# Optimization experiments

Measured on AMD Instinct MI355X. Metric: run time of the kernel, lower is better.

## Reference

```python
import jax, jax.numpy as jnp
import numpy as np

B, L, N, P = 64, 512, 321, 720   # batch, seq_len, enc_in, pred_len
E, R, CID, H = 8, 32, 32, 64     # experts, rank, channel_identity_dim, router hidden


def setup_inputs() -> dict:
    key = jax.random.key(0)
    ks = jax.random.split(key, 9)
    return {
        "x": jax.random.normal(ks[0], (B, L, N), dtype=jnp.float32),
        # per-channel identity embedding for the router
        "ident": jax.random.normal(ks[1], (N, CID), dtype=jnp.float32) * 0.02,
        # router MLP: CID -> H -> E
        "rw1": jax.random.normal(ks[2], (CID, H), dtype=jnp.float32) * (1.0 / np.sqrt(CID)),
        "rb1": jnp.zeros((H,), dtype=jnp.float32),
        "rw2": jax.random.normal(ks[3], (H, E), dtype=jnp.float32) * (1.0 / np.sqrt(H)),
        "rb2": jnp.zeros((E,), dtype=jnp.float32),
        # low-rank experts: L -> R -> P
        "w1": jax.random.normal(ks[4], (E, L, R), dtype=jnp.float32) * (1.0 / np.sqrt(L)),
        "w2": jax.random.normal(ks[5], (E, R, P), dtype=jnp.float32) * (1.0 / np.sqrt(R)),
        "b": jnp.zeros((E, P), dtype=jnp.float32),
    }


def reference(x, ident, rw1, rb1, rw2, rb2, w1, w2, b):
    # RevIN-style normalization over the time dim (torch std is unbiased, ddof=1)
    mean = jnp.mean(x, axis=1, keepdims=True)                    # [B,1,N]
    std = jnp.std(x, axis=1, keepdims=True, ddof=1) + 1e-6       # [B,1,N]
    xn = ((x - mean) / std).transpose(0, 2, 1)                   # [B,N,L]

    # per-channel MoE router (soft routing over experts)
    hidden = jax.nn.relu(ident @ rw1 + rb1)                      # [N,H]
    gate = jax.nn.softmax(hidden @ rw2 + rb2, axis=-1)           # [N,E]

    # low-rank expert projections L -> R -> P
    h = jnp.einsum('bnl,elr->bner', xn, w1)                      # [B,N,E,R]
    y = jnp.einsum('bner,erp->bnep', h, w2) + b                  # [B,N,E,P]
    y = jnp.einsum('bnep,ne->bnp', y, gate)                      # [B,N,P]

    pred = y.transpose(0, 2, 1)                                  # [B,P,N]
    return pred * std + mean
```

## Files before the change

kernel.cpp:

```cpp
#include <hip/hip_runtime.h>
#include <math.h>

#define B_ 64
#define L_ 512
#define N_ 321
#define P_ 720
#define E_ 8
#define R_ 32
#define CID_ 32
#define H_ 64
#define ER_ 256
#define KB2 288
#define HGROWS 384

typedef __attribute__((ext_vector_type(8))) short bf16x8;
typedef __attribute__((ext_vector_type(4))) float f32x4;
typedef __attribute__((ext_vector_type(8))) unsigned short u16x8;
typedef __attribute__((ext_vector_type(4))) unsigned short u16x4;

#define OFF_GATE 0
#define OFF_CS1  (N_*E_)
#define OFF_W1K  (OFF_CS1 + ER_)
#define OFF_W2X  (OFF_W1K + ER_*L_/2)
#define OFF_HG   (OFF_W2X + P_*KB2/2)

__device__ __forceinline__ unsigned short f2bf(float f) {
    unsigned u = __float_as_uint(f);
    u += 0x7fffu + ((u >> 16) & 1u);
    return (unsigned short)(u >> 16);
}
__device__ __forceinline__ float bf2f(unsigned short h) {
    return __uint_as_float(((unsigned)h) << 16);
}

__global__ void router_kernel(const float* __restrict__ ident,
                              const float* __restrict__ rw1, const float* __restrict__ rb1,
                              const float* __restrict__ rw2, const float* __restrict__ rb2,
                              float* __restrict__ gate) {
    int n = blockIdx.x;
    int t = threadIdx.x;
    __shared__ float hid[H_];
    __shared__ float lg[E_];
    float acc = rb1[t];
    #pragma unroll
    for (int c = 0; c < CID_; ++c)
        acc = fmaf(ident[n*CID_ + c], rw1[c*H_ + t], acc);
    hid[t] = fmaxf(acc, 0.f);
    __syncthreads();
    if (t < E_) {
        float a = rb2[t];
        #pragma unroll
        for (int h = 0; h < H_; ++h) a = fmaf(hid[h], rw2[h*E_ + t], a);
        lg[t] = a;
    }
    __syncthreads();
    if (t == 0) {
        float m = lg[0];
        #pragma unroll
        for (int e = 1; e < E_; ++e) m = fmaxf(m, lg[e]);
        float s = 0.f, ex[E_];
        #pragma unroll
        for (int e = 0; e < E_; ++e) { ex[e] = expf(lg[e] - m); s += ex[e]; }
        float inv = 1.f / s;
        #pragma unroll
        for (int e = 0; e < E_; ++e) gate[n*E_ + e] = ex[e] * inv;
    }
}

__global__ void prep_kernel(const float* __restrict__ w1, const float* __restrict__ w2,
                            const float* __restrict__ bias,
                            unsigned short* __restrict__ w1k, unsigned short* __restrict__ w2x,
                            float* __restrict__ cs1) {
    __shared__ float red[16][32];
    int bid = blockIdx.x, t = threadIdx.x;
    if (bid < 256) {
        int g = bid*512 + t;
        int er = g >> 9, l = g & 511;
        w1k[g] = f2bf(w1[(size_t)(er >> 5)*(L_*R_) + (size_t)l*R_ + (er & 31)]);
    } else if (bid < 256 + 720) {
        int p = bid - 256;
        if (t < KB2) {
            unsigned short v;
            if (t < ER_)            v = f2bf(w2[(size_t)t*P_ + p]);
            else if (t < ER_ + E_)  v = f2bf(bias[(size_t)(t - ER_)*P_ + p]);
            else if (t == ER_ + E_) v = 0x3f80;
            else                    v = 0;
            w2x[(size_t)p*KB2 + t] = v;
        }
    } else {
        int e = bid - 976;
        int q = t >> 5, r = t & 31;
        float s = 0.f;
        for (int l = q; l < L_; l += 16)
            s += bf2f(f2bf(w1[(size_t)e*(L_*R_) + (size_t)l*R_ + r]));
        red[q][r] = s;
        __syncthreads();
        if (q == 0) {
            #pragma unroll
            for (int qq = 1; qq < 16; ++qq) s += red[qq][r];
            cs1[e*32 + r] = s;
        }
    }
}

#define SM_XT   0
#define SM_RED  65536
#define SM_MSD  (65536+4096)
#define SM_TOT  (65536+4096+512)

__global__ __launch_bounds__(512, 4) void gemm1_kernel(
        const float* __restrict__ x, const unsigned short* __restrict__ w1k,
        const float* __restrict__ gate, const float* __restrict__ cs1,
        unsigned short* __restrict__ hg) {
    __shared__ __align__(16) char smem[SM_TOT];
    char* xTc   = smem + SM_XT;
    float* red1 = (float*)(smem + SM_RED);
    float* red2 = red1 + 512;
    float* meanS = (float*)(smem + SM_MSD);
    float* sdS   = meanS + 64;

    const int bid = blockIdx.x;
    const int xcd = bid & 7;
    const int idx = bid >> 3;
    const int b   = (xcd << 3) + idx / 6;
    const int n0  = (idx % 6) * 64;

    const int tid  = threadIdx.x;
    const int lane = tid & 63;
    const int wave = tid >> 6;
    const int l15  = lane & 15;
    const int kgrp = lane >> 4;

    const int xn = tid & 63;
    const int ks8 = tid >> 6;
    const float* xb = x + (size_t)b * L_ * N_;
    const int gn = n0 + xn;
    const bool nvalid = (gn < N_);
    const int xsw = (xn & 7) << 4;

    float s1 = 0.f, s2 = 0.f;
    #pragma unroll
    for (int c8 = 0; c8 < 8; ++c8) {
        const int k0 = ks8*64 + c8*8;
        float v[8];
        #pragma unroll
        for (int j = 0; j < 8; ++j)
            v[j] = nvalid ? xb[(size_t)(k0 + j)*N_ + gn] : 0.f;
        u16x8 pk;
        #pragma unroll
        for (int j = 0; j < 8; ++j) {
            s1 += v[j]; s2 = fmaf(v[j], v[j], s2); pk[j] = f2bf(v[j]);
        }
        *(u16x8*)(xTc + xn*1024 + ((k0*2) ^ xsw)) = pk;
    }
    red1[ks8*64 + xn] = s1;
    red2[ks8*64 + xn] = s2;
    __syncthreads();

    if (tid < 64) {
        float a = 0.f, q = 0.f;
        #pragma unroll
        for (int kk = 0; kk < 8; ++kk) { a += red1[kk*64 + tid]; q += red2[kk*64 + tid]; }
        float mean = a * (1.f/L_);
        float var = (q - (float)L_*mean*mean) * (1.f/(L_-1));
        var = fmaxf(var, 0.f);
        meanS[tid] = mean;
        sdS[tid]   = sqrtf(var) + 1e-6f;
    }
    __syncthreads();

    const unsigned short* apA = w1k + (size_t)(wave*32 + l15)*L_;
    const unsigned short* apB = w1k + (size_t)(wave*32 + 16 + l15)*L_;
    const int rsw = (l15 & 7) << 4;

    f32x4 acc[2][4];
    #pragma unroll
    for (int i = 0; i < 2; ++i)
        #pragma unroll
        for (int j = 0; j < 4; ++j) acc[i][j] = (f32x4){0.f,0.f,0.f,0.f};

    bf16x8 af[4][2];
#define LDA(s_, ks_) { af[s_][0] = *(const bf16x8*)&apA[(ks_)*32 + kgrp*8];      \
                       af[s_][1] = *(const bf16x8*)&apB[(ks_)*32 + kgrp*8]; }
    LDA(0, 0); LDA(1, 1); LDA(2, 2);
    #pragma unroll
    for (int ks = 0; ks < 16; ++ks) {
        if (ks + 3 < 16) LDA((ks + 3) & 3, ks + 3);
        const int cur = ks & 3;
        const int kb = (ks*32 + kgrp*8) * 2;
        #pragma unroll
        for (int fn = 0; fn < 4; ++fn) {
            bf16x8 bfr = *(const bf16x8*)(xTc + (fn*16 + l15)*1024 + (kb ^ rsw));
            acc[0][fn] = __builtin_amdgcn_mfma_f32_16x16x32_bf16(af[cur][0], bfr, acc[0][fn], 0, 0, 0);
            acc[1][fn] = __builtin_amdgcn_mfma_f32_16x16x32_bf16(af[cur][1], bfr, acc[1][fn], 0, 0, 0);
        }
    }
#undef LDA

    unsigned short* hgb = hg + ((size_t)b * HGROWS + n0) * KB2;
    #pragma unroll
    for (int fm = 0; fm < 2; ++fm) {
        int er0 = wave*32 + fm*16 + kgrp*4;
        int e = er0 >> 5;
        f32x4 c4 = *(const f32x4*)&cs1[er0];
        #pragma unroll
        for (int fn = 0; fn < 4; ++fn) {
            int nl = fn*16 + l15;
            int gnn = n0 + nl; if (gnn > N_-1) gnn = N_-1;
            float g = gate[gnn*E_ + e];
            float m = meanS[nl];
            u16x4 pk;
            #pragma unroll
            for (int j = 0; j < 4; ++j)
                pk[j] = f2bf(g * (acc[fm][fn][j] - m * c4[j]));
            *(u16x4*)&hgb[(size_t)nl*KB2 + er0] = pk;
        }
    }
    {
        int nl = tid >> 3, seg = tid & 7;
        int gnn = n0 + nl; if (gnn > N_-1) gnn = N_-1;
        float sd = sdS[nl], m = meanS[nl];
        u16x4 pk;
        #pragma unroll
        for (int jj = 0; jj < 4; ++jj) {
            int k = seg*4 + jj;
            float v = (k < E_) ? gate[gnn*E_ + k] * sd : ((k == E_) ? m : 0.f);
            pk[jj] = f2bf(v);
        }
        *(u16x4*)&hgb[(size_t)nl*KB2 + ER_ + seg*4] = pk;
    }
}

#define HGS 296
__global__ __launch_bounds__(512, 6) void gemm2_kernel(
        const unsigned short* __restrict__ hg, const unsigned short* __restrict__ w2x,
        float* __restrict__ out) {
    __shared__ __align__(16) char smem[64 * HGS * 2];
    unsigned short* hgL = (unsigned short*)smem;
    const int bid = blockIdx.x;
    const int xcd = bid & 7;
    const int idx = bid >> 3;
    const int b   = (xcd << 3) + idx / 36;
    const int rem = idx % 36;
    const int p0  = (rem / 6) * 128;
    const int n0  = (rem % 6) * 64;

    const int tid  = threadIdx.x;
    const int lane = tid & 63;
    const int wave = tid >> 6;
    const int l15  = lane & 15;
    const int kgrp = lane >> 4;

    const unsigned short* hgb = hg + ((size_t)b * HGROWS + n0) * KB2;
    #pragma unroll
    for (int it = 0; it < 5; ++it) {
        int c = tid + it*512;
        if (c < 64*36) {
            int row = c / 36, col = c % 36;
            *(u16x8*)&hgL[(size_t)row*HGS + col*8] =
                *(const u16x8*)&hgb[(size_t)row*KB2 + col*8];
        }
    }
    __syncthreads();

    int prow = p0 + wave*16 + l15; if (prow > P_-1) prow = P_-1;
    const unsigned short* ap = w2x + (size_t)prow*KB2;
    f32x4 o[4];
    #pragma unroll
    for (int j = 0; j < 4; ++j) o[j] = (f32x4){0.f,0.f,0.f,0.f};
    #pragma unroll
    for (int ks = 0; ks < 9; ++ks) {
        bf16x8 afr = *(const bf16x8*)&ap[ks*32 + kgrp*8];
        #pragma unroll
        for (int fn = 0; fn < 4; ++fn) {
            bf16x8 bfr = *(const bf16x8*)&hgL[(size_t)(fn*16 + l15)*HGS + ks*32 + kgrp*8];
            o[fn] = __builtin_amdgcn_mfma_f32_16x16x32_bf16(afr, bfr, o[fn], 0, 0, 0);
        }
    }
    __syncthreads();

    float* patch = (float*)smem + wave * 1088;
    #pragma unroll
    for (int fn = 0; fn < 4; ++fn)
        #pragma unroll
        for (int j = 0; j < 4; ++j)
            patch[(kgrp*4 + j)*68 + fn*16 + l15] = o[fn][j];
    const int pw0 = p0 + wave*16;
    #pragma unroll
    for (int pass = 0; pass < 4; ++pass) {
        int ploc = pass*4 + kgrp;
        f32x4 v = *(const f32x4*)&patch[ploc*68 + l15*4];
        int p = pw0 + ploc;
        int n = n0 + l15*4;
        if (p < P_) {
            float* orow = out + ((size_t)b*P_ + p)*N_;
            if (n + 3 < N_) {
                *(f32x4*)&orow[n] = v;
            } else {
                #pragma unroll
                for (int j = 0; j < 4; ++j)
                    if (n + j < N_) orow[n + j] = v[j];
            }
        }
    }
}

extern "C" void kernel_launch(void* const* d_in, const int* in_sizes, int n_in,
                              void* d_out, int out_size, void* d_ws, size_t ws_size,
                              hipStream_t stream) {
    const float* x     = (const float*)d_in[0];
    const float* ident = (const float*)d_in[1];
    const float* rw1   = (const float*)d_in[2];
    const float* rb1   = (const float*)d_in[3];
    const float* rw2   = (const float*)d_in[4];
    const float* rb2   = (const float*)d_in[5];
    const float* w1    = (const float*)d_in[6];
    const float* w2    = (const float*)d_in[7];
    const float* bias  = (const float*)d_in[8];
    float* out = (float*)d_out;
    float* ws  = (float*)d_ws;

    float* gate = ws + OFF_GATE;
    float* cs1  = ws + OFF_CS1;
    unsigned short* w1k = (unsigned short*)(ws + OFF_W1K);
    unsigned short* w2x = (unsigned short*)(ws + OFF_W2X);
    unsigned short* hg  = (unsigned short*)(ws + OFF_HG);

    router_kernel<<<N_, 64, 0, stream>>>(ident, rw1, rb1, rw2, rb2, gate);
    prep_kernel<<<256 + 720 + 8, 512, 0, stream>>>(w1, w2, bias, w1k, w2x, cs1);
    gemm1_kernel<<<dim3(384), 512, 0, stream>>>(x, w1k, gate, cs1, hg);
    gemm2_kernel<<<dim3(2304), 512, 0, stream>>>(hg, w2x, out);
}
```

Before: 67.52 us.

## Split x transpose and stats out of gemm1 into separate parallel kernels

The strided read of x, the bf16 conversion and the mean/std partial sums move out of gemm1 into a new prepx_kernel with 3072 blocks. That kernel writes a transposed bf16 copy of x plus per-chunk partial sums to workspace, and a small statred_kernel turns the partials into mean and std. gemm1 then reads B fragments straight from the global bf16 buffer instead of staging them in LDS. The aim is to spread the latency-bound strided load of x across far more blocks than the 384 gemm1 blocks could use. The cost is two extra launches and an extra global write and read of the transposed x buffer, and gemm1 fragment loads now depend on cache hits instead of LDS.

```diff
diff --git a/kernel.cpp b/kernel.cpp
--- a/kernel.cpp
+++ b/kernel.cpp
@@ -19,10 +19,15 @@
 typedef __attribute__((ext_vector_type(4))) unsigned short u16x4;
 
 #define OFF_GATE 0
-#define OFF_CS1  (N_*E_)
-#define OFF_W1K  (OFF_CS1 + ER_)
-#define OFF_W2X  (OFF_W1K + ER_*L_/2)
-#define OFF_HG   (OFF_W2X + P_*KB2/2)
+#define OFF_CS1  2568
+#define OFF_MEAN 2824
+#define OFF_SDEV 27400
+#define OFF_P1   51976
+#define OFF_P2   248584
+#define OFF_W1K  445192
+#define OFF_W2X  510728
+#define OFF_XT   614408
+#define OFF_HG   6905864
 
 __device__ __forceinline__ unsigned short f2bf(float f) {
     unsigned u = __float_as_uint(f);
@@ -103,22 +108,75 @@
     }
 }
 
-#define SM_XT   0
-#define SM_RED  65536
-#define SM_MSD  (65536+4096)
-#define SM_TOT  (65536+4096+512)
+__global__ __launch_bounds__(256) void prepx_kernel(
+        const float* __restrict__ x, unsigned short* __restrict__ xT,
+        float* __restrict__ p1, float* __restrict__ p2) {
+    const int bid = blockIdx.x;
+    const int b   = bid / 48;
+    const int rem = bid % 48;
+    const int kc  = rem >> 3;
+    const int kcc = rem / 6;
+    const int nt  = rem % 6;
+    const int n0  = nt * 64;
+    (void)kc;
+
+    const int t  = threadIdx.x;
+    const int nn = t >> 2;
+    const int q  = t & 3;
+
+    const int gn = n0 + nn;
+    const int gnc = (gn < N_) ? gn : (N_ - 1);
+    const float* xp = x + (size_t)b * L_ * N_ + gnc;
+    const int k0 = kcc*64 + q*16;
+
+    float v[16];
+    #pragma unroll
+    for (int i = 0; i < 16; ++i)
+        v[i] = xp[(size_t)(k0 + i) * N_];
+
+    float s1 = 0.f, s2 = 0.f;
+    u16x8 pk0, pk1;
+    #pragma unroll
+    for (int i = 0; i < 8; ++i) {
+        s1 += v[i]; s2 = fmaf(v[i], v[i], s2); pk0[i] = f2bf(v[i]);
+    }
+    #pragma unroll
+    for (int i = 0; i < 8; ++i) {
+        float f = v[8+i];
+        s1 += f; s2 = fmaf(f, f, s2); pk1[i] = f2bf(f);
+    }
+    unsigned short* xrow = xT + ((size_t)b*HGROWS + gn) * L_ + k0;
+    *(u16x8*)&xrow[0] = pk0;
+    *(u16x8*)&xrow[8] = pk1;
+
+    s1 += __shfl_xor(s1, 1); s1 += __shfl_xor(s1, 2);
+    s2 += __shfl_xor(s2, 1); s2 += __shfl_xor(s2, 2);
+    if (q == 0) {
+        size_t pidx = ((size_t)b*HGROWS + gn) * 8 + kcc;
+        p1[pidx] = s1;
+        p2[pidx] = s2;
+    }
+}
+
+__global__ __launch_bounds__(256) void statred_kernel(
+        const float* __restrict__ p1, const float* __restrict__ p2,
+        float* __restrict__ meanv, float* __restrict__ sdev) {
+    int id = blockIdx.x*256 + threadIdx.x;
+    float a = 0.f, qq = 0.f;
+    #pragma unroll
+    for (int kc = 0; kc < 8; ++kc) { a += p1[(size_t)id*8 + kc]; qq += p2[(size_t)id*8 + kc]; }
+    float mean = a * (1.f/L_);
+    float var = (qq - (float)L_*mean*mean) * (1.f/(L_-1));
+    var = fmaxf(var, 0.f);
+    meanv[id] = mean;
+    sdev[id]  = sqrtf(var) + 1e-6f;
+}
 
 __global__ __launch_bounds__(512, 4) void gemm1_kernel(
-        const float* __restrict__ x, const unsigned short* __restrict__ w1k,
+        const unsigned short* __restrict__ xT, const unsigned short* __restrict__ w1k,
         const float* __restrict__ gate, const float* __restrict__ cs1,
+        const float* __restrict__ meanv, const float* __restrict__ sdev,
         unsigned short* __restrict__ hg) {
-    __shared__ __align__(16) char smem[SM_TOT];
-    char* xTc   = smem + SM_XT;
-    float* red1 = (float*)(smem + SM_RED);
-    float* red2 = red1 + 512;
-    float* meanS = (float*)(smem + SM_MSD);
-    float* sdS   = meanS + 64;
-
     const int bid = blockIdx.x;
     const int xcd = bid & 7;
     const int idx = bid >> 3;
@@ -131,47 +189,9 @@
     const int l15  = lane & 15;
     const int kgrp = lane >> 4;
 
-    const int xn = tid & 63;
-    const int ks8 = tid >> 6;
-    const float* xb = x + (size_t)b * L_ * N_;
-    const int gn = n0 + xn;
-    const bool nvalid = (gn < N_);
-    const int xsw = (xn & 7) << 4;
-
-    float s1 = 0.f, s2 = 0.f;
-    #pragma unroll
-    for (int c8 = 0; c8 < 8; ++c8) {
-        const int k0 = ks8*64 + c8*8;
-        float v[8];
-        #pragma unroll
-        for (int j = 0; j < 8; ++j)
-            v[j] = nvalid ? xb[(size_t)(k0 + j)*N_ + gn] : 0.f;
-        u16x8 pk;
-        #pragma unroll
-        for (int j = 0; j < 8; ++j) {
-            s1 += v[j]; s2 = fmaf(v[j], v[j], s2); pk[j] = f2bf(v[j]);
-        }
-        *(u16x8*)(xTc + xn*1024 + ((k0*2) ^ xsw)) = pk;
-    }
-    red1[ks8*64 + xn] = s1;
-    red2[ks8*64 + xn] = s2;
-    __syncthreads();
-
-    if (tid < 64) {
-        float a = 0.f, q = 0.f;
-        #pragma unroll
-        for (int kk = 0; kk < 8; ++kk) { a += red1[kk*64 + tid]; q += red2[kk*64 + tid]; }
-        float mean = a * (1.f/L_);
-        float var = (q - (float)L_*mean*mean) * (1.f/(L_-1));
-        var = fmaxf(var, 0.f);
-        meanS[tid] = mean;
-        sdS[tid]   = sqrtf(var) + 1e-6f;
-    }
-    __syncthreads();
-
     const unsigned short* apA = w1k + (size_t)(wave*32 + l15)*L_;
     const unsigned short* apB = w1k + (size_t)(wave*32 + 16 + l15)*L_;
-    const int rsw = (l15 & 7) << 4;
+    const unsigned short* xb  = xT + ((size_t)b*HGROWS + n0) * L_;
 
     f32x4 acc[2][4];
     #pragma unroll
@@ -187,10 +207,9 @@
     for (int ks = 0; ks < 16; ++ks) {
         if (ks + 3 < 16) LDA((ks + 3) & 3, ks + 3);
         const int cur = ks & 3;
-        const int kb = (ks*32 + kgrp*8) * 2;
         #pragma unroll
         for (int fn = 0; fn < 4; ++fn) {
-            bf16x8 bfr = *(const bf16x8*)(xTc + (fn*16 + l15)*1024 + (kb ^ rsw));
+            bf16x8 bfr = *(const bf16x8*)&xb[(size_t)(fn*16 + l15)*L_ + ks*32 + kgrp*8];
             acc[0][fn] = __builtin_amdgcn_mfma_f32_16x16x32_bf16(af[cur][0], bfr, acc[0][fn], 0, 0, 0);
             acc[1][fn] = __builtin_amdgcn_mfma_f32_16x16x32_bf16(af[cur][1], bfr, acc[1][fn], 0, 0, 0);
         }
@@ -198,6 +217,8 @@
 #undef LDA
 
     unsigned short* hgb = hg + ((size_t)b * HGROWS + n0) * KB2;
+    const float* mrow = meanv + (size_t)b*HGROWS + n0;
+    const float* srow = sdev  + (size_t)b*HGROWS + n0;
     #pragma unroll
     for (int fm = 0; fm < 2; ++fm) {
         int er0 = wave*32 + fm*16 + kgrp*4;
@@ -208,7 +229,7 @@
             int nl = fn*16 + l15;
             int gnn = n0 + nl; if (gnn > N_-1) gnn = N_-1;
             float g = gate[gnn*E_ + e];
-            float m = meanS[nl];
+            float m = mrow[nl];
             u16x4 pk;
             #pragma unroll
             for (int j = 0; j < 4; ++j)
@@ -219,7 +240,7 @@
     {
         int nl = tid >> 3, seg = tid & 7;
         int gnn = n0 + nl; if (gnn > N_-1) gnn = N_-1;
-        float sd = sdS[nl], m = meanS[nl];
+        float sd = srow[nl], m = mrow[nl];
         u16x4 pk;
         #pragma unroll
         for (int jj = 0; jj < 4; ++jj) {
@@ -320,14 +341,21 @@
     float* out = (float*)d_out;
     float* ws  = (float*)d_ws;
 
-    float* gate = ws + OFF_GATE;
-    float* cs1  = ws + OFF_CS1;
+    float* gate  = ws + OFF_GATE;
+    float* cs1   = ws + OFF_CS1;
+    float* meanv = ws + OFF_MEAN;
+    float* sdev  = ws + OFF_SDEV;
+    float* p1    = ws + OFF_P1;
+    float* p2    = ws + OFF_P2;
     unsigned short* w1k = (unsigned short*)(ws + OFF_W1K);
     unsigned short* w2x = (unsigned short*)(ws + OFF_W2X);
+    unsigned short* xT  = (unsigned short*)(ws + OFF_XT);
     unsigned short* hg  = (unsigned short*)(ws + OFF_HG);
 
     router_kernel<<<N_, 64, 0, stream>>>(ident, rw1, rb1, rw2, rb2, gate);
     prep_kernel<<<256 + 720 + 8, 512, 0, stream>>>(w1, w2, bias, w1k, w2x, cs1);
-    gemm1_kernel<<<dim3(384), 512, 0, stream>>>(x, w1k, gate, cs1, hg);
+    prepx_kernel<<<3072, 256, 0, stream>>>(x, xT, p1, p2);
+    statred_kernel<<<(B_*HGROWS)/256, 256, 0, stream>>>(p1, p2, meanv, sdev);
+    gemm1_kernel<<<dim3(384), 512, 0, stream>>>(xT, w1k, gate, cs1, meanv, sdev, hg);
     gemm2_kernel<<<dim3(2304), 512, 0, stream>>>(hg, w2x, out);
 }
```

Result: slower. 108.8 us (+61.1%).

## Split stats into separate kernel and double-buffer x tiles in gemm1

Applied to the files above, without the earlier changes.

Moves the per-channel mean/std reduction out of gemm1 into a new stats_kernel, so gemm1 subtracts the mean before bf16 conversion instead of applying a column-sum correction. gemm1 now streams x through a double-buffered 32KB shared tile in four rounds, overlapping global loads with MFMA work, which also cuts its LDS footprint and could allow more resident blocks. The cs1 precompute is dropped and the w1 repack uses fewer blocks. The cost is that x is read twice (once by stats, once by gemm1) and there is one more kernel launch.

```diff
diff --git a/kernel.cpp b/kernel.cpp
--- a/kernel.cpp
+++ b/kernel.cpp
@@ -19,10 +19,11 @@
 typedef __attribute__((ext_vector_type(4))) unsigned short u16x4;
 
 #define OFF_GATE 0
-#define OFF_CS1  (N_*E_)
-#define OFF_W1K  (OFF_CS1 + ER_)
-#define OFF_W2X  (OFF_W1K + ER_*L_/2)
-#define OFF_HG   (OFF_W2X + P_*KB2/2)
+#define OFF_MEAN 2568
+#define OFF_SDEV 27144
+#define OFF_W1K  51720
+#define OFF_W2X  117256
+#define OFF_HG   220936
 
 __device__ __forceinline__ unsigned short f2bf(float f) {
     unsigned u = __float_as_uint(f);
@@ -69,16 +70,17 @@
 
 __global__ void prep_kernel(const float* __restrict__ w1, const float* __restrict__ w2,
                             const float* __restrict__ bias,
-                            unsigned short* __restrict__ w1k, unsigned short* __restrict__ w2x,
-                            float* __restrict__ cs1) {
-    __shared__ float red[16][32];
+                            unsigned short* __restrict__ w1k, unsigned short* __restrict__ w2x) {
     int bid = blockIdx.x, t = threadIdx.x;
-    if (bid < 256) {
-        int g = bid*512 + t;
-        int er = g >> 9, l = g & 511;
-        w1k[g] = f2bf(w1[(size_t)(er >> 5)*(L_*R_) + (size_t)l*R_ + (er & 31)]);
-    } else if (bid < 256 + 720) {
-        int p = bid - 256;
+    if (bid < 128) {
+        #pragma unroll
+        for (int r = 0; r < 2; ++r) {
+            int g = bid*1024 + r*512 + t;
+            int er = g >> 9, l = g & 511;
+            w1k[g] = f2bf(w1[(size_t)(er >> 5)*(L_*R_) + (size_t)l*R_ + (er & 31)]);
+        }
+    } else {
+        int p = bid - 128;
         if (t < KB2) {
             unsigned short v;
             if (t < ER_)            v = f2bf(w2[(size_t)t*P_ + p]);
@@ -87,37 +89,48 @@
             else                    v = 0;
             w2x[(size_t)p*KB2 + t] = v;
         }
-    } else {
-        int e = bid - 976;
-        int q = t >> 5, r = t & 31;
-        float s = 0.f;
-        for (int l = q; l < L_; l += 16)
-            s += bf2f(f2bf(w1[(size_t)e*(L_*R_) + (size_t)l*R_ + r]));
-        red[q][r] = s;
-        __syncthreads();
-        if (q == 0) {
-            #pragma unroll
-            for (int qq = 1; qq < 16; ++qq) s += red[qq][r];
-            cs1[e*32 + r] = s;
-        }
-    }
-}
-
-#define SM_XT   0
-#define SM_RED  65536
-#define SM_MSD  (65536+4096)
-#define SM_TOT  (65536+4096+512)
+    }
+}
+
+__global__ __launch_bounds__(512) void stats_kernel(
+        const float* __restrict__ x, float* __restrict__ meanv, float* __restrict__ sdev) {
+    __shared__ float red1[8][64], red2[8][64];
+    const int bid = blockIdx.x;
+    const int b   = bid / 6;
+    const int n0  = (bid % 6) * 64;
+    const int t   = threadIdx.x;
+    const int xn  = t & 63;
+    const int q   = t >> 6;
+    const int gn  = n0 + xn;
+    const int gnc = (gn < N_) ? gn : (N_ - 1);
+    const float* xp = x + (size_t)b*L_*N_ + gnc;
+
+    float s1 = 0.f, s2 = 0.f;
+    #pragma unroll 8
+    for (int i = 0; i < 64; ++i) {
+        float v = xp[(size_t)(q*64 + i)*N_];
+        s1 += v; s2 = fmaf(v, v, s2);
+    }
+    red1[q][xn] = s1; red2[q][xn] = s2;
+    __syncthreads();
+    if (t < 64) {
+        float a = 0.f, qq = 0.f;
+        #pragma unroll
+        for (int kk = 0; kk < 8; ++kk) { a += red1[kk][t]; qq += red2[kk][t]; }
+        float mean = a * (1.f/L_);
+        float var = (qq - (float)L_*mean*mean) * (1.f/(L_-1));
+        var = fmaxf(var, 0.f);
+        size_t id = (size_t)b*HGROWS + n0 + t;
+        meanv[id] = mean;
+        sdev[id]  = sqrtf(var) + 1e-6f;
+    }
+}
 
 __global__ __launch_bounds__(512, 4) void gemm1_kernel(
         const float* __restrict__ x, const unsigned short* __restrict__ w1k,
-        const float* __restrict__ gate, const float* __restrict__ cs1,
-        unsigned short* __restrict__ hg) {
-    __shared__ __align__(16) char smem[SM_TOT];
-    char* xTc   = smem + SM_XT;
-    float* red1 = (float*)(smem + SM_RED);
-    float* red2 = red1 + 512;
-    float* meanS = (float*)(smem + SM_MSD);
-    float* sdS   = meanS + 64;
+        const float* __restrict__ gate, const float* __restrict__ meanv,
+        const float* __restrict__ sdev, unsigned short* __restrict__ hg) {
+    __shared__ unsigned short buf[2][64][128];
 
     const int bid = blockIdx.x;
     const int xcd = bid & 7;
@@ -131,101 +144,105 @@
     const int l15  = lane & 15;
     const int kgrp = lane >> 4;
 
-    const int xn = tid & 63;
-    const int ks8 = tid >> 6;
-    const float* xb = x + (size_t)b * L_ * N_;
-    const int gn = n0 + xn;
-    const bool nvalid = (gn < N_);
-    const int xsw = (xn & 7) << 4;
-
-    float s1 = 0.f, s2 = 0.f;
-    #pragma unroll
-    for (int c8 = 0; c8 < 8; ++c8) {
-        const int k0 = ks8*64 + c8*8;
-        float v[8];
-        #pragma unroll
-        for (int j = 0; j < 8; ++j)
-            v[j] = nvalid ? xb[(size_t)(k0 + j)*N_ + gn] : 0.f;
-        u16x8 pk;
-        #pragma unroll
-        for (int j = 0; j < 8; ++j) {
-            s1 += v[j]; s2 = fmaf(v[j], v[j], s2); pk[j] = f2bf(v[j]);
-        }
-        *(u16x8*)(xTc + xn*1024 + ((k0*2) ^ xsw)) = pk;
-    }
-    red1[ks8*64 + xn] = s1;
-    red2[ks8*64 + xn] = s2;
-    __syncthreads();
-
-    if (tid < 64) {
-        float a = 0.f, q = 0.f;
-        #pragma unroll
-        for (int kk = 0; kk < 8; ++kk) { a += red1[kk*64 + tid]; q += red2[kk*64 + tid]; }
-        float mean = a * (1.f/L_);
-        float var = (q - (float)L_*mean*mean) * (1.f/(L_-1));
-        var = fmaxf(var, 0.f);
-        meanS[tid] = mean;
-        sdS[tid]   = sqrtf(var) + 1e-6f;
-    }
-    __syncthreads();
+    const int xn  = lane;
+    const int gn  = n0 + xn;
+    const int gnc = (gn < N_) ? gn : (N_ - 1);
+    const float* xp = x + (size_t)b*L_*N_ + gnc;
+    const float mean_n = meanv[(size_t)b*HGROWS + n0 + ((gn < N_) ? xn : 0)];
+    const int swz = (xn & 7) << 4;
+    char* myrow0 = (char*)&buf[0][xn][0];
+    char* myrow1 = (char*)&buf[1][xn][0];
 
     const unsigned short* apA = w1k + (size_t)(wave*32 + l15)*L_;
     const unsigned short* apB = w1k + (size_t)(wave*32 + 16 + l15)*L_;
     const int rsw = (l15 & 7) << 4;
 
+    float v[16];
     f32x4 acc[2][4];
     #pragma unroll
     for (int i = 0; i < 2; ++i)
         #pragma unroll
         for (int j = 0; j < 4; ++j) acc[i][j] = (f32x4){0.f,0.f,0.f,0.f};
 
+#define LOADV(rd_) {                                                            \
+    const int kb = (rd_)*128 + wave*16;                                         \
+    _Pragma("unroll")                                                           \
+    for (int i_ = 0; i_ < 16; ++i_)                                             \
+        v[i_] = xp[(size_t)(kb + i_)*N_]; }
+#define STOREV(rd_) {                                                           \
+    char* dst = ((rd_) & 1) ? myrow1 : myrow0;                                  \
+    u16x8 pk0, pk1;                                                             \
+    _Pragma("unroll")                                                           \
+    for (int i_ = 0; i_ < 8; ++i_)  pk0[i_] = f2bf(v[i_] - mean_n);             \
+    _Pragma("unroll")                                                           \
+    for (int i_ = 0; i_ < 8; ++i_)  pk1[i_] = f2bf(v[8+i_] - mean_n);           \
+    *(u16x8*)(dst + ((wave*32)      ^ swz)) = pk0;                              \
+    *(u16x8*)(dst + ((wave*32 + 16) ^ swz)) = pk1; }
+
+    LOADV(0);
+    STOREV(0);
+    __syncthreads();
+
     bf16x8 af[4][2];
-#define LDA(s_, ks_) { af[s_][0] = *(const bf16x8*)&apA[(ks_)*32 + kgrp*8];      \
-                       af[s_][1] = *(const bf16x8*)&apB[(ks_)*32 + kgrp*8]; }
-    LDA(0, 0); LDA(1, 1); LDA(2, 2);
-    #pragma unroll
-    for (int ks = 0; ks < 16; ++ks) {
-        if (ks + 3 < 16) LDA((ks + 3) & 3, ks + 3);
-        const int cur = ks & 3;
-        const int kb = (ks*32 + kgrp*8) * 2;
-        #pragma unroll
-        for (int fn = 0; fn < 4; ++fn) {
-            bf16x8 bfr = *(const bf16x8*)(xTc + (fn*16 + l15)*1024 + (kb ^ rsw));
-            acc[0][fn] = __builtin_amdgcn_mfma_f32_16x16x32_bf16(af[cur][0], bfr, acc[0][fn], 0, 0, 0);
-            acc[1][fn] = __builtin_amdgcn_mfma_f32_16x16x32_bf16(af[cur][1], bfr, acc[1][fn], 0, 0, 0);
-        }
+#define LDA(s_, kk_) { af[s_][0] = *(const bf16x8*)&apA[(kk_)*32 + kgrp*8];      \
+                       af[s_][1] = *(const bf16x8*)&apB[(kk_)*32 + kgrp*8]; }
+    LDA(0, 0); LDA(1, 1);
+
+    #pragma unroll
+    for (int rd = 0; rd < 4; ++rd) {
+        if (rd < 3) LOADV(rd + 1);
+        const unsigned short (*cb)[128] = buf[rd & 1];
+        #pragma unroll
+        for (int ks = 0; ks < 4; ++ks) {
+            const int kk = rd*4 + ks;
+            if (kk + 2 < 16) LDA((kk + 2) & 3, kk + 2);
+            const int cbyte = ks*64 + kgrp*16;
+            bf16x8 bfr[4];
+            #pragma unroll
+            for (int fn = 0; fn < 4; ++fn)
+                bfr[fn] = *(const bf16x8*)((const char*)&cb[fn*16 + l15][0] + (cbyte ^ rsw));
+            #pragma unroll
+            for (int fn = 0; fn < 4; ++fn) {
+                acc[0][fn] = __builtin_amdgcn_mfma_f32_16x16x32_bf16(af[kk & 3][0], bfr[fn], acc[0][fn], 0, 0, 0);
+                acc[1][fn] = __builtin_amdgcn_mfma_f32_16x16x32_bf16(af[kk & 3][1], bfr[fn], acc[1][fn], 0, 0, 0);
+            }
+        }
+        if (rd < 3) STOREV(rd + 1);
+        __syncthreads();
     }
 #undef LDA
+#undef LOADV
+#undef STOREV
 
     unsigned short* hgb = hg + ((size_t)b * HGROWS + n0) * KB2;
+    const float* mrow = meanv + (size_t)b*HGROWS + n0;
+    const float* srow = sdev  + (size_t)b*HGROWS + n0;
     #pragma unroll
     for (int fm = 0; fm < 2; ++fm) {
         int er0 = wave*32 + fm*16 + kgrp*4;
         int e = er0 >> 5;
-        f32x4 c4 = *(const f32x4*)&cs1[er0];
         #pragma unroll
         for (int fn = 0; fn < 4; ++fn) {
             int nl = fn*16 + l15;
             int gnn = n0 + nl; if (gnn > N_-1) gnn = N_-1;
             float g = gate[gnn*E_ + e];
-            float m = meanS[nl];
             u16x4 pk;
             #pragma unroll
             for (int j = 0; j < 4; ++j)
-                pk[j] = f2bf(g * (acc[fm][fn][j] - m * c4[j]));
+                pk[j] = f2bf(g * acc[fm][fn][j]);
             *(u16x4*)&hgb[(size_t)nl*KB2 + er0] = pk;
         }
     }
     {
         int nl = tid >> 3, seg = tid & 7;
         int gnn = n0 + nl; if (gnn > N_-1) gnn = N_-1;
-        float sd = sdS[nl], m = meanS[nl];
+        float sd = srow[nl], m = mrow[nl];
         u16x4 pk;
         #pragma unroll
         for (int jj = 0; jj < 4; ++jj) {
             int k = seg*4 + jj;
-            float v = (k < E_) ? gate[gnn*E_ + k] * sd : ((k == E_) ? m : 0.f);
-            pk[jj] = f2bf(v);
+            float vv = (k < E_) ? gate[gnn*E_ + k] * sd : ((k == E_) ? m : 0.f);
+            pk[jj] = f2bf(vv);
         }
         *(u16x4*)&hgb[(size_t)nl*KB2 + ER_ + seg*4] = pk;
     }
@@ -320,14 +337,16 @@
     float* out = (float*)d_out;
     float* ws  = (float*)d_ws;
 
-    float* gate = ws + OFF_GATE;
-    float* cs1  = ws + OFF_CS1;
+    float* gate  = ws + OFF_GATE;
+    float* meanv = ws + OFF_MEAN;
+    float* sdev  = ws + OFF_SDEV;
     unsigned short* w1k = (unsigned short*)(ws + OFF_W1K);
     unsigned short* w2x = (unsigned short*)(ws + OFF_W2X);
     unsigned short* hg  = (unsigned short*)(ws + OFF_HG);
 
     router_kernel<<<N_, 64, 0, stream>>>(ident, rw1, rb1, rw2, rb2, gate);
-    prep_kernel<<<256 + 720 + 8, 512, 0, stream>>>(w1, w2, bias, w1k, w2x, cs1);
-    gemm1_kernel<<<dim3(384), 512, 0, stream>>>(x, w1k, gate, cs1, hg);
+    prep_kernel<<<128 + 720, 512, 0, stream>>>(w1, w2, bias, w1k, w2x);
+    stats_kernel<<<384, 512, 0, stream>>>(x, meanv, sdev);
+    gemm1_kernel<<<dim3(384), 512, 0, stream>>>(x, w1k, gate, meanv, sdev, hg);
     gemm2_kernel<<<dim3(2304), 512, 0, stream>>>(hg, w2x, out);
 }
```

Measured after the change: 74.23 us. 1.1x slower.
